# Kernel optimization log

Measured on AMD Instinct MI355X. Metric: run time of the kernel, lower is better.

## Reference

```python
import jax, jax.numpy as jnp
import numpy as np

NEG = -1e9


def _ln(x, g, b):
    m = x.mean(-1, keepdims=True)
    v = ((x - m) ** 2).mean(-1, keepdims=True)
    return (x - m) / jnp.sqrt(v + 1e-5) * g + b


def _block(single, pair, single_mask, pair_mask,
           pa_ln_g, pa_ln_b, pa_wqkv, pa_wg, pa_wout,
           pt_ln_g, pt_ln_b, pt_w1, pt_b1, pt_w2, pt_b2,
           sa_ln_g, sa_ln_b, sa_wq, sa_wkv, sa_wb, sa_wout,
           st_ln_g, st_ln_b, st_w1, st_b1, st_w2, st_b2):
    B, L, _, D = pair.shape
    H = sa_wb.shape[1]
    hd = D // H
    scale = 1.0 / jnp.sqrt(jnp.asarray(hd, dtype=pair.dtype))
    # ---- PairUpdate: PairAttention over L*L pseudo-tokens ----
    z = _ln(pair, pa_ln_g, pa_ln_b)                       # [B,L,L,D]
    N = L * L
    qkv = (z @ pa_wqkv).reshape(B, N, 3, H, hd)
    q = qkv[:, :, 0].transpose(0, 2, 1, 3)                # [B,H,N,hd]
    k = qkv[:, :, 1].transpose(0, 2, 1, 3)
    v = qkv[:, :, 2].transpose(0, 2, 1, 3)
    attn = jnp.einsum('bhid,bhjd->bhij', q, k) * scale    # [B,H,N,N]
    pm = pair_mask.reshape(B, 1, N)
    m = pm[:, :, :, None] * pm[:, :, None, :]             # [B,1,N,N]
    attn = jnp.where(m > 0, attn, NEG)
    attn = jax.nn.softmax(attn, axis=-1)
    out = jnp.einsum('bhij,bhjd->bhid', attn, v)          # [B,H,N,hd]
    out = out.transpose(0, 2, 1, 3).reshape(B, L, L, D)
    g = jax.nn.sigmoid(z @ pa_wg)
    out = (out @ pa_wout) * g * pair_mask[..., None]
    pair = pair + out
    t = _ln(pair, pt_ln_g, pt_ln_b)
    t = jax.nn.relu(t @ pt_w1 + pt_b1) @ pt_w2 + pt_b2
    pair = pair + t * pair_mask[..., None]
    # ---- SingleUpdate: AttentionPairBias ----
    s = _ln(single, sa_ln_g, sa_ln_b)                     # [B,L,D]
    q = (s @ sa_wq).reshape(B, L, H, hd)
    kv = (s @ sa_wkv).reshape(B, L, 2, H, hd)
    k2, v2 = kv[:, :, 0], kv[:, :, 1]
    attn = jnp.einsum('bihd,bjhd->bhij', q, k2) * scale   # [B,H,L,L]
    bias = (pair @ sa_wb).transpose(0, 3, 1, 2)           # [B,H,L,L]
    attn = attn + bias
    sm = single_mask[:, None, None, :]
    attn = jnp.where(sm > 0, attn, NEG)
    attn = jax.nn.softmax(attn, axis=-1)
    out = jnp.einsum('bhij,bjhd->bihd', attn, v2).reshape(B, L, D)
    single = single + (out @ sa_wout) * single_mask[..., None]
    # single transition
    t = _ln(single, st_ln_g, st_ln_b)
    t = jax.nn.relu(t @ st_w1 + st_b1) @ st_w2 + st_b2
    single = single + t * single_mask[..., None]
    return single, pair


def setup_inputs() -> dict:
    key = jax.random.key(0)
    B, L, D, H = 1, 64, 144, 8
    ks = iter(jax.random.split(key, 40))
    def nrm(shape, scale=0.02):
        return jax.random.normal(next(ks), shape, dtype=jnp.float32) * scale
    sm = jnp.ones((B, L), jnp.float32).at[:, L - 8:].set(0.0)
    pm = sm[:, :, None] * sm[:, None, :]
    return dict(
        single=jax.random.normal(next(ks), (B, L, D), jnp.float32),
        pair=jax.random.normal(next(ks), (B, L, L, D), jnp.float32),
        single_mask=sm,
        pair_mask=pm,
        pa_ln_g=jnp.ones((D,), jnp.float32), pa_ln_b=jnp.zeros((D,), jnp.float32),
        pa_wqkv=nrm((D, 3 * D)), pa_wg=nrm((D, D)), pa_wout=nrm((D, D)),
        pt_ln_g=jnp.ones((D,), jnp.float32), pt_ln_b=jnp.zeros((D,), jnp.float32),
        pt_w1=nrm((D, 4 * D)), pt_b1=jnp.zeros((4 * D,), jnp.float32),
        pt_w2=nrm((4 * D, D)), pt_b2=jnp.zeros((D,), jnp.float32),
        sa_ln_g=jnp.ones((D,), jnp.float32), sa_ln_b=jnp.zeros((D,), jnp.float32),
        sa_wq=nrm((D, D)), sa_wkv=nrm((D, 2 * D)), sa_wb=nrm((D, H)), sa_wout=nrm((D, D)),
        st_ln_g=jnp.ones((D,), jnp.float32), st_ln_b=jnp.zeros((D,), jnp.float32),
        st_w1=nrm((D, 4 * D)), st_b1=jnp.zeros((4 * D,), jnp.float32),
        st_w2=nrm((4 * D, D)), st_b2=jnp.zeros((D,), jnp.float32),
    )


def reference(single, pair, single_mask, pair_mask,
              pa_ln_g, pa_ln_b, pa_wqkv, pa_wg, pa_wout,
              pt_ln_g, pt_ln_b, pt_w1, pt_b1, pt_w2, pt_b2,
              sa_ln_g, sa_ln_b, sa_wq, sa_wkv, sa_wb, sa_wout,
              st_ln_g, st_ln_b, st_w1, st_b1, st_w2, st_b2):
    return _block(single, pair, single_mask, pair_mask,
                  pa_ln_g, pa_ln_b, pa_wqkv, pa_wg, pa_wout,
                  pt_ln_g, pt_ln_b, pt_w1, pt_b1, pt_w2, pt_b2,
                  sa_ln_g, sa_ln_b, sa_wq, sa_wkv, sa_wb, sa_wout,
                  st_ln_g, st_ln_b, st_w1, st_b1, st_w2, st_b2)
```

## Files before the change

kernel.cpp:

```cpp
#include <hip/hip_runtime.h>
#include <hip/hip_bf16.h>

typedef __hip_bfloat16 bf16;
typedef __attribute__((ext_vector_type(8))) short short8;
typedef __attribute__((ext_vector_type(16))) float floatx16;
typedef __attribute__((ext_vector_type(4))) unsigned int uint4v;

__device__ __forceinline__ float tof(bf16 x){ return __bfloat162float(x); }
__device__ __forceinline__ float bflo(unsigned u){ return __uint_as_float(u<<16); }
__device__ __forceinline__ float bfhi(unsigned u){ return __uint_as_float(u & 0xFFFF0000u); }
__device__ __forceinline__ float ldT(const void* p, long i, bool isf){
  return isf ? ((const float*)p)[i] : tof(((const bf16*)p)[i]);
}
__device__ __forceinline__ void stT(void* p, long i, bool isf, float v){
  if (isf) ((float*)p)[i] = v; else ((bf16*)p)[i] = __float2bfloat16(v);
}

#define LL 64
#define DD 144
#define NN 4096
#define HH 8
#define HDIM 18
#define SCALE 0.23570226039551584f
#define LOG2E 1.4426950408889634f

__global__ __launch_bounds__(256) void prep_weights(const unsigned* __restrict__ smaskw,
    int* __restrict__ dflag,
    const void* __restrict__ wqkv, const void* __restrict__ wg,
    const void* __restrict__ wout, const void* __restrict__ w1, const void* __restrict__ w2,
    const void* __restrict__ swq, const void* __restrict__ swkv,
    const void* __restrict__ swout, const void* __restrict__ sw1, const void* __restrict__ sw2,
    bf16* __restrict__ F1, bf16* __restrict__ Fout, bf16* __restrict__ Fw1,
    bf16* __restrict__ Fw2, bf16* __restrict__ Fs1, bf16* __restrict__ Wtswout,
    bf16* __restrict__ Wtst1, bf16* __restrict__ Wtst2){
  bool isf = (smaskw[0] == 0x3F800000u);
  if (blockIdx.x==0 && threadIdx.x==0) dflag[0] = isf ? 4 : 2;
  long t = (long)blockIdx.x*256 + threadIdx.x;
  if (t < 82944){
    int j=t&7, lane=(int)((t>>3)&63); long tk=t>>9; int ks=tk%9, tile=tk/9;
    int col=tile*32+(lane&31); int k=ks*16+(lane>>5)*8+j;
    float v = (col<432)? ldT(wqkv,(long)k*432+col,isf) : ldT(wg,(long)k*144+(col-432),isf);
    F1[t]=__float2bfloat16(v); return;
  } t -= 82944;
  if (t < 23040){
    int j=t&7, lane=(int)((t>>3)&63); long tk=t>>9; int ks=tk%9, tile=tk/9;
    int col=tile*32+(lane&31); if (col>143) col=143;
    int k=ks*16+(lane>>5)*8+j;
    Fout[t]=__float2bfloat16(ldT(wout,(long)k*144+col,isf)); return;
  } t -= 23040;
  if (t < 82944){
    int j=t&7, lane=(int)((t>>3)&63); long tk=t>>9; int ks=tk%9, tile=tk/9;
    int col=tile*32+(lane&31); int k=ks*16+(lane>>5)*8+j;
    Fw1[t]=__float2bfloat16(ldT(w1,(long)k*576+col,isf)); return;
  } t -= 82944;
  if (t < 92160){
    int j=t&7, lane=(int)((t>>3)&63); long tk=t>>9; int ks=tk%36, tile=tk/36;
    int col=tile*32+(lane&31); if (col>143) col=143;
    int k=ks*16+(lane>>5)*8+j;
    Fw2[t]=__float2bfloat16(ldT(w2,(long)k*144+col,isf)); return;
  } t -= 92160;
  if (t < 64512){
    int j=t&7, lane=(int)((t>>3)&63); long tk=t>>9; int ks=tk%9, tile=tk/9;
    int col=tile*32+(lane&31); if (col>431) col=431;
    int k=ks*16+(lane>>5)*8+j;
    float v = (col<144)? ldT(swq,(long)k*144+col,isf) : ldT(swkv,(long)k*288+(col-144),isf);
    Fs1[t]=__float2bfloat16(v); return;
  } t -= 64512;
  if (t < 20736){ int c=t/144,k=t-(long)c*144; Wtswout[t]=__float2bfloat16(ldT(swout,(long)k*144+c,isf)); return; }
  t -= 20736;
  if (t < 82944){ int c=t/144,k=t-(long)c*144; Wtst1[t]=__float2bfloat16(ldT(sw1,(long)k*576+c,isf)); return; }
  t -= 82944;
  if (t < 82944){ int c=t/576,k=t-(long)c*576; Wtst2[t]=__float2bfloat16(ldT(sw2,(long)k*144+c,isf)); return; }
}

__global__ __launch_bounds__(256) void gemm_fused1(const int* __restrict__ df,
    const void* __restrict__ pairv, const void* __restrict__ lng, const void* __restrict__ lnb,
    const bf16* __restrict__ F1,
    const void* __restrict__ pmask,
    bf16* __restrict__ Qb, bf16* __restrict__ Kf, bf16* __restrict__ Vf,
    bf16* __restrict__ gbuf){
  __shared__ short As[64*152];
  bool isf = df[0]==4;
  int row0 = blockIdx.y*64, col0 = blockIdx.x*64;
  int tid=threadIdx.x, lane=tid&63, l31=lane&31, w=tid>>6, wr=w>>1, wc=w&1;
  int g=(lane>>5)*8;
  for (int rr=w; rr<64; rr+=4){
    long base=(long)(row0+rr)*DD;
    float e0=ldT(pairv,base+lane,isf), e1=ldT(pairv,base+lane+64,isf);
    float e2=(lane<16)?ldT(pairv,base+lane+128,isf):0.f;
    float s=e0+e1+e2;
    #pragma unroll
    for (int o=32;o;o>>=1) s += __shfl_xor(s,o);
    float mean=s*(1.f/144.f);
    float d0=e0-mean, d1=e1-mean, d2=(lane<16)?(e2-mean):0.f;
    float v=d0*d0+d1*d1+d2*d2;
    #pragma unroll
    for (int o=32;o;o>>=1) v += __shfl_xor(v,o);
    float rstd=rsqrtf(v*(1.f/144.f)+1e-5f);
    bf16 h0=__float2bfloat16(d0*rstd*ldT(lng,lane,isf)+ldT(lnb,lane,isf));
    bf16 h1=__float2bfloat16(d1*rstd*ldT(lng,lane+64,isf)+ldT(lnb,lane+64,isf));
    As[rr*152+lane]=*reinterpret_cast<short*>(&h0);
    As[rr*152+lane+64]=*reinterpret_cast<short*>(&h1);
    if (lane<16){
      bf16 h2=__float2bfloat16(d2*rstd*ldT(lng,lane+128,isf)+ldT(lnb,lane+128,isf));
      As[rr*152+lane+128]=*reinterpret_cast<short*>(&h2);
    }
  }
  __syncthreads();
  int tile = blockIdx.x*2 + wc;
  const short8* wf = (const short8*)F1;
  floatx16 acc;
  #pragma unroll
  for (int i=0;i<16;i++) acc[i]=0.f;
  #pragma unroll
  for (int ks=0; ks<9; ks++){
    short8 af = *(const short8*)&As[(l31+32*wr)*152 + ks*16 + g];
    acc = __builtin_amdgcn_mfma_f32_32x32x16_bf16(af, wf[(tile*9+ks)*64+lane], acc, 0,0,0);
  }
  int col = col0 + wc*32 + l31;
  #pragma unroll
  for (int r=0;r<16;r++){
    int row = row0 + 32*wr + (r&3)+8*(r>>2)+4*(lane>>5);
    if (col < 144){
      int hh = col/18, d = col - hh*18;
      Qb[((size_t)hh*NN+row)*32 + d] = __float2bfloat16(acc[r]*(SCALE*LOG2E));
    } else if (col < 288){
      int c2 = col-144, hh = c2/18, d = c2 - hh*18;
      int f = d>>4, rem = d&15, gs = rem>>3, j = rem&7;
      Kf[((((size_t)hh*128 + (row>>5))*2 + f)*64 + gs*32 + (row&31))*8 + j]
        = __float2bfloat16(acc[r]);
    } else if (col < 432){
      int c2 = col-288, hh = c2/18, d = c2 - hh*18;
      float pm = (ldT(pmask,row,isf)>0.f)?1.f:0.f;
      int kin = row&31, f = kin>>4, k15 = kin&15;
      int gs = (k15>>2)&1, j = (k15&3) | (((k15>>3)&1)<<2);
      Vf[((((size_t)hh*128 + (row>>5))*2 + f)*64 + gs*32 + d)*8 + j]
        = __float2bfloat16(acc[r]*pm);
    } else {
      int c2 = col-432;
      float gt = 1.f/(1.f+__expf(fminf(-acc[r],30.f)));
      gbuf[(size_t)row*DD+c2] = __float2bfloat16(gt);
    }
  }
  if (blockIdx.x==0){
    for (int t=threadIdx.x; t<64*8*7; t+=256){
      int n = row0 + t/56; int rem = t%56; int hh = rem/7, dw = rem%7 + 9;
      ((unsigned*)(Qb + ((size_t)hh*NN+n)*32))[dw] = 0;
    }
    for (int t=threadIdx.x; t<64*8; t+=256){
      int n = row0 + (t>>3), hh = t&7;
      float pm = (ldT(pmask,n,isf)>0.f)?1.f:0.f;
      int kin = n&31, f = kin>>4, k15 = kin&15;
      int gs = (k15>>2)&1, j = (k15&3) | (((k15>>3)&1)<<2);
      Vf[((((size_t)hh*128 + (n>>5))*2 + f)*64 + gs*32 + 18)*8 + j] = __float2bfloat16(pm);
    }
  }
}

__global__ __launch_bounds__(256) void pair_attn_mfma(const int* __restrict__ df,
    const bf16* __restrict__ Qb, const bf16* __restrict__ Kf,
    const bf16* __restrict__ Vf, bf16* __restrict__ aob){
  __shared__ float Comb[4][32][20];
  int h = blockIdx.x & 7, qt = blockIdx.x >> 3;
  int tid = threadIdx.x;
  int w = tid >> 6, lane = tid & 63;
  int l31 = lane & 31, gsel = lane>>5;

  const unsigned* qp = (const unsigned*)(Qb + ((size_t)h*NN + qt*32 + l31)*32);
  short8 qf0, qf1;
  #pragma unroll
  for (int j=0;j<4;j++) ((unsigned*)&qf0)[j] = qp[gsel*4+j];
  #pragma unroll
  for (int j=0;j<4;j++) ((unsigned*)&qf1)[j] = qp[8+gsel*4+j];

  floatx16 o;
  #pragma unroll
  for (int i=0;i<16;i++) o[i]=0.f;

  const short8* kf8 = (const short8*)Kf + (size_t)h*16384;
  const short8* vf8 = (const short8*)Vf + (size_t)h*16384;
  int c0 = w*32;

  short8 af0 = kf8[(c0*2+0)*64 + lane];
  short8 af1 = kf8[(c0*2+1)*64 + lane];
  short8 av0 = vf8[(c0*2+0)*64 + lane];
  short8 av1 = vf8[(c0*2+1)*64 + lane];

  for (int cc=0; cc<32; cc++){
    int cn = c0 + (cc<31 ? cc+1 : 31);
    short8 naf0 = kf8[(cn*2+0)*64 + lane];
    short8 naf1 = kf8[(cn*2+1)*64 + lane];
    short8 nav0 = vf8[(cn*2+0)*64 + lane];
    short8 nav1 = vf8[(cn*2+1)*64 + lane];

    floatx16 s;
    #pragma unroll
    for (int i=0;i<16;i++) s[i]=0.f;
    __builtin_amdgcn_s_setprio(1);
    s = __builtin_amdgcn_mfma_f32_32x32x16_bf16(af0, qf0, s, 0,0,0);
    s = __builtin_amdgcn_mfma_f32_32x32x16_bf16(af1, qf1, s, 0,0,0);
    __builtin_amdgcn_s_setprio(0);

    short8 P1, P2;
    #pragma unroll
    for (int j=0;j<4;j++){
      unsigned e0 = __float_as_uint(__builtin_amdgcn_exp2f(s[2*j]));
      unsigned e1 = __float_as_uint(__builtin_amdgcn_exp2f(s[2*j+1]));
      ((unsigned*)&P1)[j] = (e0>>16) | (e1 & 0xFFFF0000u);
      unsigned e2 = __float_as_uint(__builtin_amdgcn_exp2f(s[8+2*j]));
      unsigned e3 = __float_as_uint(__builtin_amdgcn_exp2f(s[9+2*j]));
      ((unsigned*)&P2)[j] = (e2>>16) | (e3 & 0xFFFF0000u);
    }

    __builtin_amdgcn_s_setprio(1);
    o = __builtin_amdgcn_mfma_f32_32x32x16_bf16(av0, P1, o, 0,0,0);
    o = __builtin_amdgcn_mfma_f32_32x32x16_bf16(av1, P2, o, 0,0,0);
    __builtin_amdgcn_s_setprio(0);

    af0=naf0; af1=naf1; av0=nav0; av1=nav1;
  }

  #pragma unroll
  for (int r=0;r<16;r++){
    int d = (r&3) + 8*(r>>2) + 4*gsel;
    if (d < 20) Comb[w][l31][d] = o[r];
  }
  __syncthreads();
  for (int t=tid; t<32*HDIM; t+=256){
    int q = t/HDIM, d = t-q*HDIM;
    float num = Comb[0][q][d]+Comb[1][q][d]+Comb[2][q][d]+Comb[3][q][d];
    float den = Comb[0][q][18]+Comb[1][q][18]+Comb[2][q][18]+Comb[3][q][18];
    aob[(size_t)(qt*32+q)*DD + h*HDIM + d] = __float2bfloat16(num/fmaxf(den,1e-20f));
  }
}

__global__ __launch_bounds__(512) void pair_tail(const int* __restrict__ df,
    const bf16* __restrict__ aob, const bf16* __restrict__ gbuf,
    const void* __restrict__ pairv, const void* __restrict__ pmaskv,
    const bf16* __restrict__ Fout, const void* __restrict__ ptln_g, const void* __restrict__ ptln_b,
    const bf16* __restrict__ Fw1, const void* __restrict__ b1v,
    const bf16* __restrict__ Fw2, const void* __restrict__ b2v,
    const void* __restrict__ wb, void* __restrict__ outP, long outOff,
    float* __restrict__ biasb){
  __shared__ __align__(16) char smem[16384];
  float* p1  = (float*)smem;
  short* ts  = (short*)(smem + 4608);
  short* hh_ = (short*)(smem + 7040);
  float* outv = (float*)(smem + 7040);

  bool isf = df[0]==4;
  int tid=threadIdx.x, lane=tid&63, l31=lane&31, gsel=lane>>5, g=gsel*8;
  int w=tid>>6;
  int lrow = l31 & 7;
  int r0 = blockIdx.x*8;
  const short8* foutf = (const short8*)Fout;
  const short8* fw1f  = (const short8*)Fw1;
  const short8* fw2f  = (const short8*)Fw2;

  for (int t=tid; t<8*72; t+=512){
    int m=t/72, dw=t%72;
    ((unsigned*)ts)[m*76+dw] = ((const unsigned*)(aob + (size_t)(r0+m)*144))[dw];
  }
  __syncthreads();

  for (int tile=w; tile<5; tile+=8){
    int c0=tile*32;
    floatx16 acc;
    #pragma unroll
    for (int i=0;i<16;i++) acc[i]=0.f;
    #pragma unroll
    for (int ks=0; ks<9; ks++){
      short8 af = *(const short8*)&ts[lrow*152 + ks*16 + g];
      acc = __builtin_amdgcn_mfma_f32_32x32x16_bf16(af, foutf[(tile*9+ks)*64+lane], acc, 0,0,0);
    }
    if (c0+l31 < 144){
      #pragma unroll
      for (int r=0;r<16;r++){
        int row=(r&3)+8*(r>>2)+4*gsel;
        if (row<8) p1[row*144 + c0+l31] = acc[r];
      }
    }
  }
  __syncthreads();
  for (int t=tid; t<8*144; t+=512){
    int row=t/144; int col=t-row*144;
    long gidx=(long)(r0+row)*144 + col;
    float pm = (ldT(pmaskv, r0+row, isf)>0.f)?1.f:0.f;
    p1[t] = ldT(pairv,gidx,isf) + p1[t]*tof(gbuf[gidx])*pm;
  }
  __syncthreads();
  if (w < 8){
    int rr = w;
    float e0=p1[rr*144+lane], e1=p1[rr*144+lane+64], e2=(lane<16)?p1[rr*144+lane+128]:0.f;
    float s=e0+e1+e2;
    #pragma unroll
    for (int o=32;o;o>>=1) s += __shfl_xor(s,o);
    float mean=s*(1.f/144.f);
    float d0=e0-mean, d1=e1-mean, d2=(lane<16)?(e2-mean):0.f;
    float v=d0*d0+d1*d1+d2*d2;
    #pragma unroll
    for (int o=32;o;o>>=1) v += __shfl_xor(v,o);
    float rstd=rsqrtf(v*(1.f/144.f)+1e-5f);
    bf16 h0 = __float2bfloat16(d0*rstd*ldT(ptln_g,lane,isf)    + ldT(ptln_b,lane,isf));
    bf16 h1 = __float2bfloat16(d1*rstd*ldT(ptln_g,lane+64,isf) + ldT(ptln_b,lane+64,isf));
    ts[rr*152+lane]    = *reinterpret_cast<short*>(&h0);
    ts[rr*152+lane+64] = *reinterpret_cast<short*>(&h1);
    if (lane<16){
      bf16 h2 = __float2bfloat16(d2*rstd*ldT(ptln_g,lane+128,isf) + ldT(ptln_b,lane+128,isf));
      ts[rr*152+lane+128] = *reinterpret_cast<short*>(&h2);
    }
  }
  __syncthreads();
  for (int tile=w; tile<18; tile+=8){
    int c0=tile*32, colB=c0+l31;
    floatx16 acc;
    #pragma unroll
    for (int i=0;i<16;i++) acc[i]=0.f;
    #pragma unroll
    for (int ks=0; ks<9; ks++){
      short8 af = *(const short8*)&ts[lrow*152 + ks*16 + g];
      acc = __builtin_amdgcn_mfma_f32_32x32x16_bf16(af, fw1f[(tile*9+ks)*64+lane], acc, 0,0,0);
    }
    float bb = ldT(b1v,colB,isf);
    #pragma unroll
    for (int r=0;r<16;r++){
      int row=(r&3)+8*(r>>2)+4*gsel;
      if (row<8){
        bf16 hv = __float2bfloat16(fmaxf(acc[r]+bb,0.f));
        hh_[row*584 + colB] = *reinterpret_cast<short*>(&hv);
      }
    }
  }
  __syncthreads();
  floatx16 fin; int fc0 = -1;
  for (int tile=w; tile<5; tile+=8){
    int c0=tile*32;
    int colB=c0+l31; if (colB>143) colB=143;
    floatx16 acc;
    #pragma unroll
    for (int i=0;i<16;i++) acc[i]=0.f;
    #pragma unroll
    for (int ks=0; ks<36; ks++){
      short8 af = *(const short8*)&hh_[lrow*584 + ks*16 + g];
      acc = __builtin_amdgcn_mfma_f32_32x32x16_bf16(af, fw2f[(tile*36+ks)*64+lane], acc, 0,0,0);
    }
    float bb = ldT(b2v,colB,isf);
    #pragma unroll
    for (int r=0;r<16;r++){
      int row=(r&3)+8*(r>>2)+4*gsel;
      float val = 0.f;
      if (row<8){
        float pm = (ldT(pmaskv, r0+row, isf)>0.f)?1.f:0.f;
        val = p1[row*144 + colB] + (acc[r]+bb)*pm;
        if (c0+l31 < 144)
          stT(outP, outOff + (long)(r0+row)*144 + c0+l31, isf, val);
      }
      fin[r]=val;
    }
    fc0 = c0;
  }
  __syncthreads();
  if (fc0 >= 0 && fc0+l31 < 144){
    #pragma unroll
    for (int r=0;r<16;r++){
      int row=(r&3)+8*(r>>2)+4*gsel;
      if (row<8) outv[row*144 + fc0+l31] = fin[r];
    }
  }
  __syncthreads();
  {
    int n = tid>>3, hb = tid&7;
    if (n < 8){
      float acc=0.f;
      #pragma unroll 4
      for (int k=0;k<144;k++) acc += outv[n*144+k]*ldT(wb,k*8+hb,isf);
      biasb[(size_t)(r0+n)*8+hb]=acc;
    }
  }
}

__global__ __launch_bounds__(256) void gemm_s1(const int* __restrict__ df,
    const void* __restrict__ single, const void* __restrict__ g, const void* __restrict__ b,
    const bf16* __restrict__ Fs1,
    bf16* __restrict__ q_sb, bf16* __restrict__ kv_sb){
  __shared__ short As[64*152];
  bool isf = df[0]==4;
  int tid=threadIdx.x, lane=tid&63, l31=lane&31, w=tid>>6, wr=w>>1, wc=w&1;
  int gg=(lane>>5)*8;
  for (int rr=w; rr<64; rr+=4){
    long base=(long)rr*DD;
    float e0=ldT(single,base+lane,isf), e1=ldT(single,base+lane+64,isf);
    float e2=(lane<16)?ldT(single,base+lane+128,isf):0.f;
    float s=e0+e1+e2;
    #pragma unroll
    for (int o=32;o;o>>=1) s += __shfl_xor(s,o);
    float mean=s*(1.f/144.f);
    float d0=e0-mean, d1=e1-mean, d2=(lane<16)?(e2-mean):0.f;
    float v=d0*d0+d1*d1+d2*d2;
    #pragma unroll
    for (int o=32;o;o>>=1) v += __shfl_xor(v,o);
    float rstd=rsqrtf(v*(1.f/144.f)+1e-5f);
    bf16 h0=__float2bfloat16(d0*rstd*ldT(g,lane,isf)+ldT(b,lane,isf));
    bf16 h1=__float2bfloat16(d1*rstd*ldT(g,lane+64,isf)+ldT(b,lane+64,isf));
    As[rr*152+lane]=*reinterpret_cast<short*>(&h0);
    As[rr*152+lane+64]=*reinterpret_cast<short*>(&h1);
    if (lane<16){
      bf16 h2=__float2bfloat16(d2*rstd*ldT(g,lane+128,isf)+ldT(b,lane+128,isf));
      As[rr*152+lane+128]=*reinterpret_cast<short*>(&h2);
    }
  }
  __syncthreads();
  int tile = blockIdx.x*2 + wc;
  const short8* wf = (const short8*)Fs1;
  floatx16 acc;
  #pragma unroll
  for (int i=0;i<16;i++) acc[i]=0.f;
  #pragma unroll
  for (int ks=0; ks<9; ks++){
    short8 af = *(const short8*)&As[(l31+32*wr)*152 + ks*16 + gg];
    acc = __builtin_amdgcn_mfma_f32_32x32x16_bf16(af, wf[(tile*9+ks)*64+lane], acc, 0,0,0);
  }
  int col = tile*32 + l31;
  if (col < 432){
    #pragma unroll
    for (int r=0;r<16;r++){
      int row = 32*wr + (r&3)+8*(r>>2)+4*(lane>>5);
      if (col<144) q_sb[(size_t)row*DD+col] = __float2bfloat16(acc[r]);
      else kv_sb[(size_t)row*288+(col-144)] = __float2bfloat16(acc[r]);
    }
  }
}

__global__ __launch_bounds__(256) void single_tail(const int* __restrict__ df,
    const void* __restrict__ single, const bf16* __restrict__ q_sb,
    const bf16* __restrict__ kv_sb, const float* __restrict__ biasb,
    const void* __restrict__ smask, const bf16* __restrict__ Wtswout,
    const void* __restrict__ stln_g, const void* __restrict__ stln_b,
    const bf16* __restrict__ Wtst1, const void* __restrict__ st_b1,
    const bf16* __restrict__ Wtst2, const void* __restrict__ st_b2,
    void* __restrict__ outS){
  bool isf = df[0]==4;
  __shared__ __align__(16) short kvs[64*288];
  __shared__ float pexp[8][64];
  __shared__ float tot[8];
  __shared__ __align__(16) float bb[512];
  __shared__ float qs[DD], as_[DD], s1[DD], tss[DD], hs[576];
  __shared__ float mr[2];
  int n = blockIdx.x, tid = threadIdx.x;
  {
    const uint4v* src = (const uint4v*)kv_sb;
    uint4v* dst = (uint4v*)kvs;
    for (int t=tid; t<2304; t+=256) dst[t] = src[t];
  }
  if (tid<DD) qs[tid] = tof(q_sb[(size_t)n*DD+tid]);
  {
    const uint4v* src = (const uint4v*)(biasb + (size_t)n*512);
    uint4v* dst = (uint4v*)bb;
    if (tid<128) dst[tid] = src[tid];
  }
  __syncthreads();
  #pragma unroll
  for (int pp=0; pp<2; pp++){
    int pi = tid + pp*256;
    int h = pi>>6, j = pi&63;
    const unsigned* kr = (const unsigned*)&kvs[j*288 + h*HDIM];
    float s=0.f;
    #pragma unroll
    for (int i=0;i<9;i++){
      unsigned u = kr[i];
      s += qs[h*HDIM+2*i]*bflo(u) + qs[h*HDIM+2*i+1]*bfhi(u);
    }
    s = fminf(s*SCALE + bb[j*8+h], 30.f);
    pexp[h][j] = (ldT(smask,j,isf)>0.f) ? __expf(s) : 0.f;
  }
  __syncthreads();
  if (tid<64){
    int h=tid>>3, j0=(tid&7)*8;
    float t2=0.f;
    #pragma unroll
    for (int j=0;j<8;j++) t2 += pexp[h][j0+j];
    #pragma unroll
    for (int o=4;o;o>>=1) t2 += __shfl_xor(t2,o);
    if ((tid&7)==0) tot[h] = fmaxf(t2,1e-20f);
  }
  __syncthreads();
  if (tid<DD){
    int h = tid/HDIM;
    float acc=0.f;
    #pragma unroll 8
    for (int j=0;j<64;j++){
      unsigned u = ((unsigned)(unsigned short)kvs[j*288 + 144 + tid])<<16;
      acc += pexp[h][j]*__uint_as_float(u);
    }
    as_[tid] = acc/tot[h];
  }
  __syncthreads();
  float sm = ldT(smask,n,isf);
  if (tid<DD){
    const uint4v* wr = (const uint4v*)(Wtswout + (size_t)tid*DD);
    float a=0.f;
    #pragma unroll 3
    for (int kw=0; kw<18; kw++){
      uint4v u = wr[kw];
      a += as_[8*kw+0]*bflo(u[0]) + as_[8*kw+1]*bfhi(u[0])
         + as_[8*kw+2]*bflo(u[1]) + as_[8*kw+3]*bfhi(u[1])
         + as_[8*kw+4]*bflo(u[2]) + as_[8*kw+5]*bfhi(u[2])
         + as_[8*kw+6]*bflo(u[3]) + as_[8*kw+7]*bfhi(u[3]);
    }
    s1[tid] = ldT(single,(long)n*DD+tid,isf) + a*sm;
  }
  __syncthreads();
  if (tid < 64){
    float e0 = s1[tid], e1 = s1[tid+64], e2 = (tid<16)?s1[tid+128]:0.f;
    float s = e0+e1+e2;
    #pragma unroll
    for (int o=32;o;o>>=1) s += __shfl_xor(s,o);
    float mean = s*(1.f/144.f);
    float d0=e0-mean, d1=e1-mean, d2=(tid<16)?(e2-mean):0.f;
    float v = d0*d0+d1*d1+d2*d2;
    #pragma unroll
    for (int o=32;o;o>>=1) v += __shfl_xor(v,o);
    if (tid==0){ mr[0]=mean; mr[1]=rsqrtf(v*(1.f/144.f)+1e-5f); }
  }
  __syncthreads();
  if (tid<DD) tss[tid] = (s1[tid]-mr[0])*mr[1]*ldT(stln_g,tid,isf) + ldT(stln_b,tid,isf);
  __syncthreads();
  for (int c=tid;c<576;c+=256){
    const uint4v* wr = (const uint4v*)(Wtst1 + (size_t)c*DD);
    float a=ldT(st_b1,c,isf);
    #pragma unroll 3
    for (int kw=0; kw<18; kw++){
      uint4v u = wr[kw];
      a += tss[8*kw+0]*bflo(u[0]) + tss[8*kw+1]*bfhi(u[0])
         + tss[8*kw+2]*bflo(u[1]) + tss[8*kw+3]*bfhi(u[1])
         + tss[8*kw+4]*bflo(u[2]) + tss[8*kw+5]*bfhi(u[2])
         + tss[8*kw+6]*bflo(u[3]) + tss[8*kw+7]*bfhi(u[3]);
    }
    hs[c]=fmaxf(a,0.f);
  }
  __syncthreads();
  if (tid<DD){
    const uint4v* wr = (const uint4v*)(Wtst2 + (size_t)tid*576);
    float a=ldT(st_b2,tid,isf);
    #pragma unroll 4
    for (int kw=0; kw<72; kw++){
      uint4v u = wr[kw];
      a += hs[8*kw+0]*bflo(u[0]) + hs[8*kw+1]*bfhi(u[0])
         + hs[8*kw+2]*bflo(u[1]) + hs[8*kw+3]*bfhi(u[1])
         + hs[8*kw+4]*bflo(u[2]) + hs[8*kw+5]*bfhi(u[2])
         + hs[8*kw+6]*bflo(u[3]) + hs[8*kw+7]*bfhi(u[3]);
    }
    stT(outS,(long)n*DD+tid,isf, s1[tid] + a*sm);
  }
}

extern "C" void kernel_launch(void* const* d_in, const int* in_sizes, int n_in,
                              void* d_out, int out_size, void* d_ws, size_t ws_size,
                              hipStream_t stream) {
  char* wsb = (char*)d_ws;
  int*   dflag = (int*)wsb;
  bf16*  F1     = (bf16*)(wsb + 16);
  bf16*  Fout   = F1 + 82944;
  bf16*  Fw1    = Fout + 23040;
  bf16*  Fw2    = Fw1 + 82944;
  bf16*  Fs1    = Fw2 + 92160;
  bf16*  Wtswout= Fs1 + 64512;
  bf16*  Wtst1  = Wtswout + 20736;
  bf16*  Wtst2  = Wtst1 + 82944;
  bf16*  Qb   = Wtst2 + 82944;
  bf16*  Kf   = Qb + (size_t)HH*NN*32;
  bf16*  Vf   = Kf + (size_t)HH*131072;
  bf16*  gbuf = Vf + (size_t)HH*131072;
  bf16*  aob  = gbuf + (size_t)NN*DD;
  float* biasb= (float*)(aob + (size_t)NN*DD);
  bf16*  q_sb = (bf16*)(biasb + NN*8);
  bf16*  kv_sb= q_sb + LL*DD;

  const long OUTP_OFF = (long)LL*DD;

  prep_weights<<<2079,256,0,stream>>>((const unsigned*)d_in[2], dflag,
      d_in[6], d_in[7], d_in[8], d_in[11], d_in[13],
      d_in[17], d_in[18], d_in[20], d_in[23], d_in[25],
      F1, Fout, Fw1, Fw2, Fs1, Wtswout, Wtst1, Wtst2);

  gemm_fused1<<<dim3(9,64),256,0,stream>>>(dflag, d_in[1], d_in[4], d_in[5], F1, d_in[3],
                                           Qb, Kf, Vf, gbuf);
  pair_attn_mfma<<<1024,256,0,stream>>>(dflag, Qb, Kf, Vf, aob);
  pair_tail<<<512,512,0,stream>>>(dflag, aob, gbuf, d_in[1], d_in[3],
                                  Fout, d_in[9], d_in[10], Fw1, d_in[12],
                                  Fw2, d_in[14], d_in[19], d_out, OUTP_OFF, biasb);

  gemm_s1<<<dim3(7,1),256,0,stream>>>(dflag, d_in[0], d_in[15], d_in[16], Fs1, q_sb, kv_sb);
  single_tail<<<LL,256,0,stream>>>(dflag, d_in[0], q_sb, kv_sb, biasb, d_in[2],
                                   Wtswout, d_in[21], d_in[22], Wtst1, d_in[24],
                                   Wtst2, d_in[26], d_out);
  (void)in_sizes; (void)n_in; (void)out_size; (void)ws_size;
}
```

Baseline: 239.1 us.

## Fuse single-LN QKV GEMM into pair GEMM launch, widen pair_tail to 32 rows

The standalone gemm_s1 kernel is folded into gemm_fused1 as an extra grid row, which removes one kernel launch. pair_tail now processes 32 rows per block instead of 8, so the 32-row MFMA tiles are fully used rather than mostly padded, and it launches 128 blocks with more shared memory each. The single_tail dot products are split into two accumulators to shorten dependency chains. The costs are lower parallelism in pair_tail (fewer blocks, 64KB LDS each, which limits occupancy) and some extra branching in gemm_fused1.

```diff
diff --git a/kernel.cpp b/kernel.cpp
--- a/kernel.cpp
+++ b/kernel.cpp
@@ -78,12 +78,63 @@
     const bf16* __restrict__ F1,
     const void* __restrict__ pmask,
     bf16* __restrict__ Qb, bf16* __restrict__ Kf, bf16* __restrict__ Vf,
-    bf16* __restrict__ gbuf){
+    bf16* __restrict__ gbuf,
+    const void* __restrict__ singlev, const void* __restrict__ sag, const void* __restrict__ sab,
+    const bf16* __restrict__ Fs1,
+    bf16* __restrict__ q_sb, bf16* __restrict__ kv_sb){
   __shared__ short As[64*152];
   bool isf = df[0]==4;
-  int row0 = blockIdx.y*64, col0 = blockIdx.x*64;
   int tid=threadIdx.x, lane=tid&63, l31=lane&31, w=tid>>6, wr=w>>1, wc=w&1;
   int g=(lane>>5)*8;
+
+  if (blockIdx.y == 64){
+    if (blockIdx.x >= 7) return;
+    for (int rr=w; rr<64; rr+=4){
+      long base=(long)rr*DD;
+      float e0=ldT(singlev,base+lane,isf), e1=ldT(singlev,base+lane+64,isf);
+      float e2=(lane<16)?ldT(singlev,base+lane+128,isf):0.f;
+      float s=e0+e1+e2;
+      #pragma unroll
+      for (int o=32;o;o>>=1) s += __shfl_xor(s,o);
+      float mean=s*(1.f/144.f);
+      float d0=e0-mean, d1=e1-mean, d2=(lane<16)?(e2-mean):0.f;
+      float v=d0*d0+d1*d1+d2*d2;
+      #pragma unroll
+      for (int o=32;o;o>>=1) v += __shfl_xor(v,o);
+      float rstd=rsqrtf(v*(1.f/144.f)+1e-5f);
+      bf16 h0=__float2bfloat16(d0*rstd*ldT(sag,lane,isf)+ldT(sab,lane,isf));
+      bf16 h1=__float2bfloat16(d1*rstd*ldT(sag,lane+64,isf)+ldT(sab,lane+64,isf));
+      As[rr*152+lane]=*reinterpret_cast<short*>(&h0);
+      As[rr*152+lane+64]=*reinterpret_cast<short*>(&h1);
+      if (lane<16){
+        bf16 h2=__float2bfloat16(d2*rstd*ldT(sag,lane+128,isf)+ldT(sab,lane+128,isf));
+        As[rr*152+lane+128]=*reinterpret_cast<short*>(&h2);
+      }
+    }
+    __syncthreads();
+    int tile = blockIdx.x*2 + wc;
+    const short8* wf = (const short8*)Fs1;
+    floatx16 acc;
+    #pragma unroll
+    for (int i=0;i<16;i++) acc[i]=0.f;
+    #pragma unroll
+    for (int ks=0; ks<9; ks++){
+      short8 af = *(const short8*)&As[(l31+32*wr)*152 + ks*16 + g];
+      acc = __builtin_amdgcn_mfma_f32_32x32x16_bf16(af, wf[(tile*9+ks)*64+lane], acc, 0,0,0);
+    }
+    int col = tile*32 + l31;
+    if (col < 432){
+      #pragma unroll
+      for (int r=0;r<16;r++){
+        int row = 32*wr + (r&3)+8*(r>>2)+4*(lane>>5);
+        if (col<144) q_sb[(size_t)row*DD+col] = __float2bfloat16(acc[r]);
+        else kv_sb[(size_t)row*288+(col-144)] = __float2bfloat16(acc[r]);
+      }
+    }
+    return;
+  }
+
+  int row0 = blockIdx.y*64, col0 = blockIdx.x*64;
   for (int rr=w; rr<64; rr+=4){
     long base=(long)(row0+rr)*DD;
     float e0=ldT(pairv,base+lane,isf), e1=ldT(pairv,base+lane+64,isf);
@@ -242,22 +293,21 @@
     const bf16* __restrict__ Fw2, const void* __restrict__ b2v,
     const void* __restrict__ wb, void* __restrict__ outP, long outOff,
     float* __restrict__ biasb){
-  __shared__ __align__(16) char smem[16384];
+  __shared__ __align__(16) char smem[65536];
   float* p1  = (float*)smem;
-  short* ts  = (short*)(smem + 4608);
-  short* hh_ = (short*)(smem + 7040);
-  float* outv = (float*)(smem + 7040);
+  short* ts  = (short*)(smem + 18432);
+  short* hh_ = (short*)(smem + 28160);
+  float* outv = (float*)(smem + 28160);
 
   bool isf = df[0]==4;
   int tid=threadIdx.x, lane=tid&63, l31=lane&31, gsel=lane>>5, g=gsel*8;
   int w=tid>>6;
-  int lrow = l31 & 7;
-  int r0 = blockIdx.x*8;
+  int r0 = blockIdx.x*32;
   const short8* foutf = (const short8*)Fout;
   const short8* fw1f  = (const short8*)Fw1;
   const short8* fw2f  = (const short8*)Fw2;
 
-  for (int t=tid; t<8*72; t+=512){
+  for (int t=tid; t<32*72; t+=512){
     int m=t/72, dw=t%72;
     ((unsigned*)ts)[m*76+dw] = ((const unsigned*)(aob + (size_t)(r0+m)*144))[dw];
   }
@@ -270,27 +320,26 @@
     for (int i=0;i<16;i++) acc[i]=0.f;
     #pragma unroll
     for (int ks=0; ks<9; ks++){
-      short8 af = *(const short8*)&ts[lrow*152 + ks*16 + g];
+      short8 af = *(const short8*)&ts[l31*152 + ks*16 + g];
       acc = __builtin_amdgcn_mfma_f32_32x32x16_bf16(af, foutf[(tile*9+ks)*64+lane], acc, 0,0,0);
     }
     if (c0+l31 < 144){
       #pragma unroll
       for (int r=0;r<16;r++){
         int row=(r&3)+8*(r>>2)+4*gsel;
-        if (row<8) p1[row*144 + c0+l31] = acc[r];
+        p1[row*144 + c0+l31] = acc[r];
       }
     }
   }
   __syncthreads();
-  for (int t=tid; t<8*144; t+=512){
+  for (int t=tid; t<32*144; t+=512){
     int row=t/144; int col=t-row*144;
     long gidx=(long)(r0+row)*144 + col;
     float pm = (ldT(pmaskv, r0+row, isf)>0.f)?1.f:0.f;
     p1[t] = ldT(pairv,gidx,isf) + p1[t]*tof(gbuf[gidx])*pm;
   }
   __syncthreads();
-  if (w < 8){
-    int rr = w;
+  for (int rr=w; rr<32; rr+=8){
     float e0=p1[rr*144+lane], e1=p1[rr*144+lane+64], e2=(lane<16)?p1[rr*144+lane+128]:0.f;
     float s=e0+e1+e2;
     #pragma unroll
@@ -318,17 +367,15 @@
     for (int i=0;i<16;i++) acc[i]=0.f;
     #pragma unroll
     for (int ks=0; ks<9; ks++){
-      short8 af = *(const short8*)&ts[lrow*152 + ks*16 + g];
+      short8 af = *(const short8*)&ts[l31*152 + ks*16 + g];
       acc = __builtin_amdgcn_mfma_f32_32x32x16_bf16(af, fw1f[(tile*9+ks)*64+lane], acc, 0,0,0);
     }
     float bb = ldT(b1v,colB,isf);
     #pragma unroll
     for (int r=0;r<16;r++){
       int row=(r&3)+8*(r>>2)+4*gsel;
-      if (row<8){
-        bf16 hv = __float2bfloat16(fmaxf(acc[r]+bb,0.f));
-        hh_[row*584 + colB] = *reinterpret_cast<short*>(&hv);
-      }
+      bf16 hv = __float2bfloat16(fmaxf(acc[r]+bb,0.f));
+      hh_[row*584 + colB] = *reinterpret_cast<short*>(&hv);
     }
   }
   __syncthreads();
@@ -341,20 +388,17 @@
     for (int i=0;i<16;i++) acc[i]=0.f;
     #pragma unroll
     for (int ks=0; ks<36; ks++){
-      short8 af = *(const short8*)&hh_[lrow*584 + ks*16 + g];
+      short8 af = *(const short8*)&hh_[l31*584 + ks*16 + g];
       acc = __builtin_amdgcn_mfma_f32_32x32x16_bf16(af, fw2f[(tile*36+ks)*64+lane], acc, 0,0,0);
     }
     float bb = ldT(b2v,colB,isf);
     #pragma unroll
     for (int r=0;r<16;r++){
       int row=(r&3)+8*(r>>2)+4*gsel;
-      float val = 0.f;
-      if (row<8){
-        float pm = (ldT(pmaskv, r0+row, isf)>0.f)?1.f:0.f;
-        val = p1[row*144 + colB] + (acc[r]+bb)*pm;
-        if (c0+l31 < 144)
-          stT(outP, outOff + (long)(r0+row)*144 + c0+l31, isf, val);
-      }
+      float pm = (ldT(pmaskv, r0+row, isf)>0.f)?1.f:0.f;
+      float val = p1[row*144 + colB] + (acc[r]+bb)*pm;
+      if (c0+l31 < 144)
+        stT(outP, outOff + (long)(r0+row)*144 + c0+l31, isf, val);
       fin[r]=val;
     }
     fc0 = c0;
@@ -364,70 +408,16 @@
     #pragma unroll
     for (int r=0;r<16;r++){
       int row=(r&3)+8*(r>>2)+4*gsel;
-      if (row<8) outv[row*144 + fc0+l31] = fin[r];
-    }
-  }
-  __syncthreads();
-  {
+      outv[row*144 + fc0+l31] = fin[r];
+    }
+  }
+  __syncthreads();
+  if (tid < 256){
     int n = tid>>3, hb = tid&7;
-    if (n < 8){
-      float acc=0.f;
-      #pragma unroll 4
-      for (int k=0;k<144;k++) acc += outv[n*144+k]*ldT(wb,k*8+hb,isf);
-      biasb[(size_t)(r0+n)*8+hb]=acc;
-    }
-  }
-}
-
-__global__ __launch_bounds__(256) void gemm_s1(const int* __restrict__ df,
-    const void* __restrict__ single, const void* __restrict__ g, const void* __restrict__ b,
-    const bf16* __restrict__ Fs1,
-    bf16* __restrict__ q_sb, bf16* __restrict__ kv_sb){
-  __shared__ short As[64*152];
-  bool isf = df[0]==4;
-  int tid=threadIdx.x, lane=tid&63, l31=lane&31, w=tid>>6, wr=w>>1, wc=w&1;
-  int gg=(lane>>5)*8;
-  for (int rr=w; rr<64; rr+=4){
-    long base=(long)rr*DD;
-    float e0=ldT(single,base+lane,isf), e1=ldT(single,base+lane+64,isf);
-    float e2=(lane<16)?ldT(single,base+lane+128,isf):0.f;
-    float s=e0+e1+e2;
-    #pragma unroll
-    for (int o=32;o;o>>=1) s += __shfl_xor(s,o);
-    float mean=s*(1.f/144.f);
-    float d0=e0-mean, d1=e1-mean, d2=(lane<16)?(e2-mean):0.f;
-    float v=d0*d0+d1*d1+d2*d2;
-    #pragma unroll
-    for (int o=32;o;o>>=1) v += __shfl_xor(v,o);
-    float rstd=rsqrtf(v*(1.f/144.f)+1e-5f);
-    bf16 h0=__float2bfloat16(d0*rstd*ldT(g,lane,isf)+ldT(b,lane,isf));
-    bf16 h1=__float2bfloat16(d1*rstd*ldT(g,lane+64,isf)+ldT(b,lane+64,isf));
-    As[rr*152+lane]=*reinterpret_cast<short*>(&h0);
-    As[rr*152+lane+64]=*reinterpret_cast<short*>(&h1);
-    if (lane<16){
-      bf16 h2=__float2bfloat16(d2*rstd*ldT(g,lane+128,isf)+ldT(b,lane+128,isf));
-      As[rr*152+lane+128]=*reinterpret_cast<short*>(&h2);
-    }
-  }
-  __syncthreads();
-  int tile = blockIdx.x*2 + wc;
-  const short8* wf = (const short8*)Fs1;
-  floatx16 acc;
-  #pragma unroll
-  for (int i=0;i<16;i++) acc[i]=0.f;
-  #pragma unroll
-  for (int ks=0; ks<9; ks++){
-    short8 af = *(const short8*)&As[(l31+32*wr)*152 + ks*16 + gg];
-    acc = __builtin_amdgcn_mfma_f32_32x32x16_bf16(af, wf[(tile*9+ks)*64+lane], acc, 0,0,0);
-  }
-  int col = tile*32 + l31;
-  if (col < 432){
-    #pragma unroll
-    for (int r=0;r<16;r++){
-      int row = 32*wr + (r&3)+8*(r>>2)+4*(lane>>5);
-      if (col<144) q_sb[(size_t)row*DD+col] = __float2bfloat16(acc[r]);
-      else kv_sb[(size_t)row*288+(col-144)] = __float2bfloat16(acc[r]);
-    }
+    float acc=0.f;
+    #pragma unroll 4
+    for (int k=0;k<144;k++) acc += outv[n*144+k]*ldT(wb,k*8+hb,isf);
+    biasb[(size_t)(r0+n)*8+hb]=acc;
   }
 }
 
@@ -486,28 +476,34 @@
   __syncthreads();
   if (tid<DD){
     int h = tid/HDIM;
-    float acc=0.f;
+    float a0=0.f, a1=0.f;
     #pragma unroll 8
-    for (int j=0;j<64;j++){
-      unsigned u = ((unsigned)(unsigned short)kvs[j*288 + 144 + tid])<<16;
-      acc += pexp[h][j]*__uint_as_float(u);
-    }
-    as_[tid] = acc/tot[h];
+    for (int j=0;j<64;j+=2){
+      unsigned u0 = ((unsigned)(unsigned short)kvs[j*288 + 144 + tid])<<16;
+      unsigned u1 = ((unsigned)(unsigned short)kvs[(j+1)*288 + 144 + tid])<<16;
+      a0 += pexp[h][j]*__uint_as_float(u0);
+      a1 += pexp[h][j+1]*__uint_as_float(u1);
+    }
+    as_[tid] = (a0+a1)/tot[h];
   }
   __syncthreads();
   float sm = ldT(smask,n,isf);
   if (tid<DD){
     const uint4v* wr = (const uint4v*)(Wtswout + (size_t)tid*DD);
-    float a=0.f;
+    float a0=0.f, a1=0.f;
     #pragma unroll 3
-    for (int kw=0; kw<18; kw++){
-      uint4v u = wr[kw];
-      a += as_[8*kw+0]*bflo(u[0]) + as_[8*kw+1]*bfhi(u[0])
-         + as_[8*kw+2]*bflo(u[1]) + as_[8*kw+3]*bfhi(u[1])
-         + as_[8*kw+4]*bflo(u[2]) + as_[8*kw+5]*bfhi(u[2])
-         + as_[8*kw+6]*bflo(u[3]) + as_[8*kw+7]*bfhi(u[3]);
-    }
-    s1[tid] = ldT(single,(long)n*DD+tid,isf) + a*sm;
+    for (int kw=0; kw<18; kw+=2){
+      uint4v u = wr[kw], u2 = wr[kw+1];
+      a0 += as_[8*kw+0]*bflo(u[0]) + as_[8*kw+1]*bfhi(u[0])
+          + as_[8*kw+2]*bflo(u[1]) + as_[8*kw+3]*bfhi(u[1])
+          + as_[8*kw+4]*bflo(u[2]) + as_[8*kw+5]*bfhi(u[2])
+          + as_[8*kw+6]*bflo(u[3]) + as_[8*kw+7]*bfhi(u[3]);
+      a1 += as_[8*kw+8]*bflo(u2[0]) + as_[8*kw+9]*bfhi(u2[0])
+          + as_[8*kw+10]*bflo(u2[1]) + as_[8*kw+11]*bfhi(u2[1])
+          + as_[8*kw+12]*bflo(u2[2]) + as_[8*kw+13]*bfhi(u2[2])
+          + as_[8*kw+14]*bflo(u2[3]) + as_[8*kw+15]*bfhi(u2[3]);
+    }
+    s1[tid] = ldT(single,(long)n*DD+tid,isf) + (a0+a1)*sm;
   }
   __syncthreads();
   if (tid < 64){
@@ -527,30 +523,38 @@
   __syncthreads();
   for (int c=tid;c<576;c+=256){
     const uint4v* wr = (const uint4v*)(Wtst1 + (size_t)c*DD);
-    float a=ldT(st_b1,c,isf);
+    float a0=ldT(st_b1,c,isf), a1=0.f;
     #pragma unroll 3
-    for (int kw=0; kw<18; kw++){
-      uint4v u = wr[kw];
-      a += tss[8*kw+0]*bflo(u[0]) + tss[8*kw+1]*bfhi(u[0])
-         + tss[8*kw+2]*bflo(u[1]) + tss[8*kw+3]*bfhi(u[1])
-         + tss[8*kw+4]*bflo(u[2]) + tss[8*kw+5]*bfhi(u[2])
-         + tss[8*kw+6]*bflo(u[3]) + tss[8*kw+7]*bfhi(u[3]);
-    }
-    hs[c]=fmaxf(a,0.f);
+    for (int kw=0; kw<18; kw+=2){
+      uint4v u = wr[kw], u2 = wr[kw+1];
+      a0 += tss[8*kw+0]*bflo(u[0]) + tss[8*kw+1]*bfhi(u[0])
+          + tss[8*kw+2]*bflo(u[1]) + tss[8*kw+3]*bfhi(u[1])
+          + tss[8*kw+4]*bflo(u[2]) + tss[8*kw+5]*bfhi(u[2])
+          + tss[8*kw+6]*bflo(u[3]) + tss[8*kw+7]*bfhi(u[3]);
+      a1 += tss[8*kw+8]*bflo(u2[0]) + tss[8*kw+9]*bfhi(u2[0])
+          + tss[8*kw+10]*bflo(u2[1]) + tss[8*kw+11]*bfhi(u2[1])
+          + tss[8*kw+12]*bflo(u2[2]) + tss[8*kw+13]*bfhi(u2[2])
+          + tss[8*kw+14]*bflo(u2[3]) + tss[8*kw+15]*bfhi(u2[3]);
+    }
+    hs[c]=fmaxf(a0+a1,0.f);
   }
   __syncthreads();
   if (tid<DD){
     const uint4v* wr = (const uint4v*)(Wtst2 + (size_t)tid*576);
-    float a=ldT(st_b2,tid,isf);
+    float a0=ldT(st_b2,tid,isf), a1=0.f;
     #pragma unroll 4
-    for (int kw=0; kw<72; kw++){
-      uint4v u = wr[kw];
-      a += hs[8*kw+0]*bflo(u[0]) + hs[8*kw+1]*bfhi(u[0])
-         + hs[8*kw+2]*bflo(u[1]) + hs[8*kw+3]*bfhi(u[1])
-         + hs[8*kw+4]*bflo(u[2]) + hs[8*kw+5]*bfhi(u[2])
-         + hs[8*kw+6]*bflo(u[3]) + hs[8*kw+7]*bfhi(u[3]);
-    }
-    stT(outS,(long)n*DD+tid,isf, s1[tid] + a*sm);
+    for (int kw=0; kw<72; kw+=2){
+      uint4v u = wr[kw], u2 = wr[kw+1];
+      a0 += hs[8*kw+0]*bflo(u[0]) + hs[8*kw+1]*bfhi(u[0])
+          + hs[8*kw+2]*bflo(u[1]) + hs[8*kw+3]*bfhi(u[1])
+          + hs[8*kw+4]*bflo(u[2]) + hs[8*kw+5]*bfhi(u[2])
+          + hs[8*kw+6]*bflo(u[3]) + hs[8*kw+7]*bfhi(u[3]);
+      a1 += hs[8*kw+8]*bflo(u2[0]) + hs[8*kw+9]*bfhi(u2[0])
+          + hs[8*kw+10]*bflo(u2[1]) + hs[8*kw+11]*bfhi(u2[1])
+          + hs[8*kw+12]*bflo(u2[2]) + hs[8*kw+13]*bfhi(u2[2])
+          + hs[8*kw+14]*bflo(u2[3]) + hs[8*kw+15]*bfhi(u2[3]);
+    }
+    stT(outS,(long)n*DD+tid,isf, s1[tid] + (a0+a1)*sm);
   }
 }
 
@@ -583,14 +587,13 @@
       d_in[17], d_in[18], d_in[20], d_in[23], d_in[25],
       F1, Fout, Fw1, Fw2, Fs1, Wtswout, Wtst1, Wtst2);
 
-  gemm_fused1<<<dim3(9,64),256,0,stream>>>(dflag, d_in[1], d_in[4], d_in[5], F1, d_in[3],
-                                           Qb, Kf, Vf, gbuf);
+  gemm_fused1<<<dim3(9,65),256,0,stream>>>(dflag, d_in[1], d_in[4], d_in[5], F1, d_in[3],
+                                           Qb, Kf, Vf, gbuf,
+                                           d_in[0], d_in[15], d_in[16], Fs1, q_sb, kv_sb);
   pair_attn_mfma<<<1024,256,0,stream>>>(dflag, Qb, Kf, Vf, aob);
-  pair_tail<<<512,512,0,stream>>>(dflag, aob, gbuf, d_in[1], d_in[3],
+  pair_tail<<<128,512,0,stream>>>(dflag, aob, gbuf, d_in[1], d_in[3],
                                   Fout, d_in[9], d_in[10], Fw1, d_in[12],
                                   Fw2, d_in[14], d_in[19], d_out, OUTP_OFF, biasb);
-
-  gemm_s1<<<dim3(7,1),256,0,stream>>>(dflag, d_in[0], d_in[15], d_in[16], Fs1, q_sb, kv_sb);
   single_tail<<<LL,256,0,stream>>>(dflag, d_in[0], q_sb, kv_sb, biasb, d_in[2],
                                    Wtswout, d_in[21], d_in[22], Wtst1, d_in[24],
                                    Wtst2, d_in[26], d_out);
```

Measured after the change: 225.2 us. 5.8% less time.
